# Performance work log

Hardware: AMD Instinct MI355X
Metric: run time of the kernel (lower is better)

The kernel has to match this reference:

```python
import jax, jax.numpy as jnp
import numpy as np

D_MODEL = 256
NCODES = 32


def setup_inputs() -> dict:
    key = jax.random.key(0)
    k1, k2 = jax.random.split(key)
    B, L = 64, 2048
    rev_repr = jax.random.normal(k1, (B, L, D_MODEL), dtype=jnp.float32)
    # xavier_normal for Linear(256 -> ncodes): std = sqrt(2/(fan_in+fan_out))
    std = (2.0 / (D_MODEL + NCODES)) ** 0.5
    W_codes = jax.random.normal(k2, (NCODES, D_MODEL), dtype=jnp.float32) * std
    return {"rev_repr": rev_repr, "W_codes": W_codes}


def reference(rev_repr, W_codes):
    # scores: (B, L, ncodes) = rev_repr @ W_codes.T
    scores = jnp.einsum('bld,kd->blk', rev_repr, W_codes)
    # softmax over the L (sequence) dimension, dim=1
    wts = jax.nn.softmax(scores, axis=1)
    # fused weighted-sum pooling: (B, ncodes, 256) — avoids (B,L,ncodes,256) intermediate
    contexts = jnp.einsum('blk,bld->bkd', wts, rev_repr)
    return contexts
```

## Files before the change

### kernel.cpp

```cpp
#include <hip/hip_runtime.h>
#include <math.h>

#define BATCH 64
#define LSEQ 2048
#define DMOD 256
#define KC 32
#define LCHUNK 128
#define NCH 16
#define LS 32
#define NSUB 4
#define PD 264
#define PT 40
#define PP 36

typedef __bf16 bf16x4 __attribute__((ext_vector_type(4)));
typedef __bf16 bf16x8 __attribute__((ext_vector_type(8)));
typedef float f32x4 __attribute__((ext_vector_type(4)));

union FragU {
  uint4 u;
  uint2 h[2];
  bf16x8 b;
};

__global__ __launch_bounds__(256, 4) void fused_pool_kernel(
    const float* __restrict__ rev, const float* __restrict__ W,
    float* __restrict__ cPartial, float* __restrict__ zPartial) {
  __shared__ __align__(16) __bf16 sRev[LS * PD];
  __shared__ __align__(16) __bf16 sRevT[DMOD * PT];
  __shared__ __align__(16) __bf16 sP[KC * PP];
  __shared__ float sZw[4][16];

  const int tid = threadIdx.x;
  const int b = blockIdx.y;
  const int lc = blockIdx.x;
  const int lbase = lc * LCHUNK;
  const int lane = tid & 63;
  const int wave = tid >> 6;
  const int col = lane & 15;
  const int quad = lane >> 4;
  const int Mt = wave & 1;
  const int Nt = wave >> 1;
  const int tp = tid & 127;
  const int th = tid >> 7;

  bf16x8 wfrag[8];
  {
    const float* wrow = W + (Nt * 16 + col) * DMOD + quad * 8;
#pragma unroll
    for (int ks = 0; ks < 8; ++ks) {
      float4 a = *(const float4*)(wrow + ks * 32);
      float4 c = *(const float4*)(wrow + ks * 32 + 4);
      bf16x8 f = {(__bf16)a.x, (__bf16)a.y, (__bf16)a.z, (__bf16)a.w,
                  (__bf16)c.x, (__bf16)c.y, (__bf16)c.z, (__bf16)c.w};
      wfrag[ks] = f;
    }
  }

  for (int rep = 0; rep < 2; ++rep) {
    f32x4 acc2[8];
#pragma unroll
    for (int i = 0; i < 8; ++i) acc2[i] = (f32x4){0.f, 0.f, 0.f, 0.f};
    float zl = 0.f;

#pragma unroll
    for (int i = 0; i < 8; ++i) {
      int slot = tid + 256 * i;
      int r = slot >> 6, c4 = slot & 63;
      float4 v = *(const float4*)(rev + ((size_t)b * LSEQ + lbase + r) * DMOD + c4 * 4);
      bf16x4 hh = {(__bf16)v.x, (__bf16)v.y, (__bf16)v.z, (__bf16)v.w};
      *(bf16x4*)(&sRev[r * PD + c4 * 4]) = hh;
    }
    __syncthreads();

    for (int sub = 0; sub < NSUB; ++sub) {
#pragma unroll
      for (int s2 = 0; s2 < 2; ++s2) {
        uint tmp[8];
#pragma unroll
        for (int j = 0; j < 8; ++j) {
          int ll = 16 * th + 8 * s2 + j;
          tmp[j] = *(const uint*)(&sRev[ll * PD + 2 * tp]);
        }
        uint lo[4], hi[4];
#pragma unroll
        for (int i = 0; i < 4; ++i) {
          lo[i] = (tmp[2 * i] & 0xffffu) | (tmp[2 * i + 1] << 16);
          hi[i] = (tmp[2 * i] >> 16) | (tmp[2 * i + 1] & 0xffff0000u);
        }
        uint4 vlo = {lo[0], lo[1], lo[2], lo[3]};
        uint4 vhi = {hi[0], hi[1], hi[2], hi[3]};
        *(uint4*)(&sRevT[(2 * tp) * PT + 16 * th + 8 * s2]) = vlo;
        *(uint4*)(&sRevT[(2 * tp + 1) * PT + 16 * th + 8 * s2]) = vhi;
      }

      f32x4 acc1 = {0.f, 0.f, 0.f, 0.f};
#pragma unroll
      for (int ks = 0; ks < 8; ++ks) {
        FragU af;
        af.u = *(const uint4*)(&sRev[(Mt * 16 + col) * PD + ks * 32 + quad * 8]);
        acc1 = __builtin_amdgcn_mfma_f32_16x16x32_bf16(af.b, wfrag[ks], acc1, 0, 0, 0);
      }
      {
        bf16x4 ph;
#pragma unroll
        for (int reg = 0; reg < 4; ++reg) {
          float p = __expf(acc1[reg]);
          ph[reg] = (__bf16)p;
          zl += (float)ph[reg];
        }
        *(bf16x4*)(&sP[(Nt * 16 + col) * PP + Mt * 16 + quad * 4]) = ph;
      }
      __syncthreads();

      FragU pa;
      pa.h[0] = *(const uint2*)(&sP[(Mt * 16 + col) * PP + quad * 8]);
      pa.h[1] = *(const uint2*)(&sP[(Mt * 16 + col) * PP + quad * 8 + 4]);
#pragma unroll
      for (int nt = 0; nt < 8; ++nt) {
        int d = (Nt * 8 + nt) * 16 + col;
        FragU bb;
        bb.u = *(const uint4*)(&sRevT[d * PT + quad * 8]);
        acc2[nt] = __builtin_amdgcn_mfma_f32_16x16x32_bf16(pa.b, bb.b, acc2[nt], 0, 0, 0);
      }
      if (sub + 1 < NSUB) {
        const int l1 = lbase + (sub + 1) * LS;
#pragma unroll
        for (int i = 0; i < 8; ++i) {
          int slot = tid + 256 * i;
          int r = slot >> 6, c4 = slot & 63;
          float4 v = *(const float4*)(rev + ((size_t)b * LSEQ + l1 + r) * DMOD + c4 * 4);
          bf16x4 hh = {(__bf16)v.x, (__bf16)v.y, (__bf16)v.z, (__bf16)v.w};
          *(bf16x4*)(&sRev[r * PD + c4 * 4]) = hh;
        }
        __syncthreads();
      }
    }

    float zz = zl;
    zz += __shfl_xor(zz, 16, 64);
    zz += __shfl_xor(zz, 32, 64);
    if (quad == 0) sZw[wave][col] = zz;
    __syncthreads();
    if (tid < KC) {
      int Ntt = tid >> 4, c = tid & 15;
      zPartial[((size_t)b * NCH + lc) * KC + tid] = sZw[2 * Ntt][c] + sZw[2 * Ntt + 1][c];
    }
    float* dst = cPartial + (((size_t)b * NCH + lc) * KC) * DMOD;
#pragma unroll
    for (int nt = 0; nt < 8; ++nt) {
      int d = (Nt * 8 + nt) * 16 + col;
#pragma unroll
      for (int reg = 0; reg < 4; ++reg) {
        int k = Mt * 16 + quad * 4 + reg;
        dst[k * DMOD + d] = acc2[nt][reg];
      }
    }
    __syncthreads();
  }
}

__global__ __launch_bounds__(256) void reduce_kernel(
    const float* __restrict__ cPartial, const float* __restrict__ zPartial,
    float* __restrict__ out) {
  int idx = blockIdx.x * 256 + threadIdx.x;
  int b = idx >> 11;
  int k = (idx >> 6) & 31;
  float4 s = {0.f, 0.f, 0.f, 0.f};
  float z = 0.f;
#pragma unroll
  for (int lcc = 0; lcc < NCH; ++lcc) {
    const float4 v = *(const float4*)(cPartial +
                                      ((((size_t)b * NCH + lcc) * KC + k) << 8) +
                                      ((idx & 63) << 2));
    s.x += v.x; s.y += v.y; s.z += v.z; s.w += v.w;
    z += zPartial[((size_t)b * NCH + lcc) * KC + k];
  }
  float zi = 1.0f / z;
  float4 o = {s.x * zi, s.y * zi, s.z * zi, s.w * zi};
  *(float4*)(out + ((size_t)idx << 2)) = o;
}

extern "C" void kernel_launch(void* const* d_in, const int* in_sizes, int n_in,
                              void* d_out, int out_size, void* d_ws,
                              size_t ws_size, hipStream_t stream) {
  const float* rev = (const float*)d_in[0];
  const float* W = (const float*)d_in[1];
  float* out = (float*)d_out;

  float* ws = (float*)d_ws;
  float* cPartial = ws;
  float* zPartial = cPartial + (size_t)BATCH * NCH * KC * DMOD;

  fused_pool_kernel<<<dim3(NCH, BATCH), dim3(256), 0, stream>>>(rev, W, cPartial,
                                                                zPartial);
  reduce_kernel<<<dim3(512), dim3(256), 0, stream>>>(cPartial, zPartial, out);
}
```

Before: 233.0 us.

## Use 512-thread blocks with 64-row subtiles and halve partial chunks

The fused pooling kernel now runs 512-thread blocks that each process a 256-row L chunk as four 64-row subtiles, instead of 256-thread blocks looping twice over 128-row chunks. The wave-to-tile mapping is reworked: 8 waves compute the scores tile, and the context MFMA now takes a K=64 reduction in two steps per output tile. NCH drops from 16 to 8, which halves the partial-sum writes and the work in the reduce kernel. In exchange it uses more shared memory and registers per block and launches fewer, larger blocks, which may lower occupancy.

```diff
diff --git a/kernel.cpp b/kernel.cpp
--- a/kernel.cpp
+++ b/kernel.cpp
@@ -5,13 +5,13 @@
 #define LSEQ 2048
 #define DMOD 256
 #define KC 32
-#define LCHUNK 128
-#define NCH 16
-#define LS 32
+#define LCH 256
+#define NCH 8
+#define LS 64
 #define NSUB 4
 #define PD 264
-#define PT 40
-#define PP 36
+#define PT 72
+#define PP 72
 
 typedef __bf16 bf16x4 __attribute__((ext_vector_type(4)));
 typedef __bf16 bf16x8 __attribute__((ext_vector_type(8)));
@@ -23,30 +23,32 @@
   bf16x8 b;
 };
 
-__global__ __launch_bounds__(256, 4) void fused_pool_kernel(
+__global__ __launch_bounds__(512, 4) void fused_pool_kernel(
     const float* __restrict__ rev, const float* __restrict__ W,
     float* __restrict__ cPartial, float* __restrict__ zPartial) {
   __shared__ __align__(16) __bf16 sRev[LS * PD];
   __shared__ __align__(16) __bf16 sRevT[DMOD * PT];
   __shared__ __align__(16) __bf16 sP[KC * PP];
-  __shared__ float sZw[4][16];
+  __shared__ float sZw[8][16];
 
   const int tid = threadIdx.x;
   const int b = blockIdx.y;
   const int lc = blockIdx.x;
-  const int lbase = lc * LCHUNK;
+  const int lbase = lc * LCH;
   const int lane = tid & 63;
   const int wave = tid >> 6;
   const int col = lane & 15;
   const int quad = lane >> 4;
-  const int Mt = wave & 1;
-  const int Nt = wave >> 1;
+  const int Mt1 = wave & 3;
+  const int Nt1 = wave >> 2;
+  const int Mt2 = wave & 1;
+  const int Dt = wave >> 1;
   const int tp = tid & 127;
   const int th = tid >> 7;
 
   bf16x8 wfrag[8];
   {
-    const float* wrow = W + (Nt * 16 + col) * DMOD + quad * 8;
+    const float* wrow = W + (Nt1 * 16 + col) * DMOD + quad * 8;
 #pragma unroll
     for (int ks = 0; ks < 8; ++ks) {
       float4 a = *(const float4*)(wrow + ks * 32);
@@ -57,106 +59,108 @@
     }
   }
 
-  for (int rep = 0; rep < 2; ++rep) {
-    f32x4 acc2[8];
-#pragma unroll
-    for (int i = 0; i < 8; ++i) acc2[i] = (f32x4){0.f, 0.f, 0.f, 0.f};
-    float zl = 0.f;
-
-#pragma unroll
-    for (int i = 0; i < 8; ++i) {
-      int slot = tid + 256 * i;
-      int r = slot >> 6, c4 = slot & 63;
-      float4 v = *(const float4*)(rev + ((size_t)b * LSEQ + lbase + r) * DMOD + c4 * 4);
-      bf16x4 hh = {(__bf16)v.x, (__bf16)v.y, (__bf16)v.z, (__bf16)v.w};
-      *(bf16x4*)(&sRev[r * PD + c4 * 4]) = hh;
+  f32x4 acc2[4];
+#pragma unroll
+  for (int i = 0; i < 4; ++i) acc2[i] = (f32x4){0.f, 0.f, 0.f, 0.f};
+  float zl = 0.f;
+
+#pragma unroll
+  for (int i = 0; i < 8; ++i) {
+    int slot = tid + 512 * i;
+    int r = slot >> 6, c4 = slot & 63;
+    float4 v = *(const float4*)(rev + ((size_t)b * LSEQ + lbase + r) * DMOD + c4 * 4);
+    bf16x4 hh = {(__bf16)v.x, (__bf16)v.y, (__bf16)v.z, (__bf16)v.w};
+    *(bf16x4*)(&sRev[r * PD + c4 * 4]) = hh;
+  }
+  __syncthreads();
+
+  for (int sub = 0; sub < NSUB; ++sub) {
+#pragma unroll
+    for (int s2 = 0; s2 < 2; ++s2) {
+      uint tmp[8];
+#pragma unroll
+      for (int j = 0; j < 8; ++j) {
+        int ll = 16 * th + 8 * s2 + j;
+        tmp[j] = *(const uint*)(&sRev[ll * PD + 2 * tp]);
+      }
+      uint lo[4], hi[4];
+#pragma unroll
+      for (int i = 0; i < 4; ++i) {
+        lo[i] = (tmp[2 * i] & 0xffffu) | (tmp[2 * i + 1] << 16);
+        hi[i] = (tmp[2 * i] >> 16) | (tmp[2 * i + 1] & 0xffff0000u);
+      }
+      uint4 vlo = {lo[0], lo[1], lo[2], lo[3]};
+      uint4 vhi = {hi[0], hi[1], hi[2], hi[3]};
+      *(uint4*)(&sRevT[(2 * tp) * PT + 16 * th + 8 * s2]) = vlo;
+      *(uint4*)(&sRevT[(2 * tp + 1) * PT + 16 * th + 8 * s2]) = vhi;
+    }
+
+    f32x4 acc1 = {0.f, 0.f, 0.f, 0.f};
+#pragma unroll
+    for (int ks = 0; ks < 8; ++ks) {
+      FragU af;
+      af.u = *(const uint4*)(&sRev[(Mt1 * 16 + col) * PD + ks * 32 + quad * 8]);
+      acc1 = __builtin_amdgcn_mfma_f32_16x16x32_bf16(af.b, wfrag[ks], acc1, 0, 0, 0);
+    }
+    {
+      bf16x4 ph;
+#pragma unroll
+      for (int reg = 0; reg < 4; ++reg) {
+        float p = __expf(acc1[reg]);
+        ph[reg] = (__bf16)p;
+        zl += (float)ph[reg];
+      }
+      *(bf16x4*)(&sP[(Nt1 * 16 + col) * PP + Mt1 * 16 + quad * 4]) = ph;
     }
     __syncthreads();
 
-    for (int sub = 0; sub < NSUB; ++sub) {
-#pragma unroll
-      for (int s2 = 0; s2 < 2; ++s2) {
-        uint tmp[8];
-#pragma unroll
-        for (int j = 0; j < 8; ++j) {
-          int ll = 16 * th + 8 * s2 + j;
-          tmp[j] = *(const uint*)(&sRev[ll * PD + 2 * tp]);
-        }
-        uint lo[4], hi[4];
-#pragma unroll
-        for (int i = 0; i < 4; ++i) {
-          lo[i] = (tmp[2 * i] & 0xffffu) | (tmp[2 * i + 1] << 16);
-          hi[i] = (tmp[2 * i] >> 16) | (tmp[2 * i + 1] & 0xffff0000u);
-        }
-        uint4 vlo = {lo[0], lo[1], lo[2], lo[3]};
-        uint4 vhi = {hi[0], hi[1], hi[2], hi[3]};
-        *(uint4*)(&sRevT[(2 * tp) * PT + 16 * th + 8 * s2]) = vlo;
-        *(uint4*)(&sRevT[(2 * tp + 1) * PT + 16 * th + 8 * s2]) = vhi;
-      }
-
-      f32x4 acc1 = {0.f, 0.f, 0.f, 0.f};
-#pragma unroll
-      for (int ks = 0; ks < 8; ++ks) {
-        FragU af;
-        af.u = *(const uint4*)(&sRev[(Mt * 16 + col) * PD + ks * 32 + quad * 8]);
-        acc1 = __builtin_amdgcn_mfma_f32_16x16x32_bf16(af.b, wfrag[ks], acc1, 0, 0, 0);
-      }
-      {
-        bf16x4 ph;
-#pragma unroll
-        for (int reg = 0; reg < 4; ++reg) {
-          float p = __expf(acc1[reg]);
-          ph[reg] = (__bf16)p;
-          zl += (float)ph[reg];
-        }
-        *(bf16x4*)(&sP[(Nt * 16 + col) * PP + Mt * 16 + quad * 4]) = ph;
+    FragU pa[2];
+#pragma unroll
+    for (int s = 0; s < 2; ++s)
+      pa[s].u = *(const uint4*)(&sP[(Mt2 * 16 + col) * PP + s * 32 + quad * 8]);
+#pragma unroll
+    for (int t = 0; t < 4; ++t) {
+      int drow = (Dt * 4 + t) * 16 + col;
+#pragma unroll
+      for (int s = 0; s < 2; ++s) {
+        FragU bb;
+        bb.u = *(const uint4*)(&sRevT[drow * PT + s * 32 + quad * 8]);
+        acc2[t] = __builtin_amdgcn_mfma_f32_16x16x32_bf16(pa[s].b, bb.b, acc2[t], 0, 0, 0);
+      }
+    }
+    if (sub + 1 < NSUB) {
+      const int l1 = lbase + (sub + 1) * LS;
+#pragma unroll
+      for (int i = 0; i < 8; ++i) {
+        int slot = tid + 512 * i;
+        int r = slot >> 6, c4 = slot & 63;
+        float4 v = *(const float4*)(rev + ((size_t)b * LSEQ + l1 + r) * DMOD + c4 * 4);
+        bf16x4 hh = {(__bf16)v.x, (__bf16)v.y, (__bf16)v.z, (__bf16)v.w};
+        *(bf16x4*)(&sRev[r * PD + c4 * 4]) = hh;
       }
       __syncthreads();
-
-      FragU pa;
-      pa.h[0] = *(const uint2*)(&sP[(Mt * 16 + col) * PP + quad * 8]);
-      pa.h[1] = *(const uint2*)(&sP[(Mt * 16 + col) * PP + quad * 8 + 4]);
-#pragma unroll
-      for (int nt = 0; nt < 8; ++nt) {
-        int d = (Nt * 8 + nt) * 16 + col;
-        FragU bb;
-        bb.u = *(const uint4*)(&sRevT[d * PT + quad * 8]);
-        acc2[nt] = __builtin_amdgcn_mfma_f32_16x16x32_bf16(pa.b, bb.b, acc2[nt], 0, 0, 0);
-      }
-      if (sub + 1 < NSUB) {
-        const int l1 = lbase + (sub + 1) * LS;
-#pragma unroll
-        for (int i = 0; i < 8; ++i) {
-          int slot = tid + 256 * i;
-          int r = slot >> 6, c4 = slot & 63;
-          float4 v = *(const float4*)(rev + ((size_t)b * LSEQ + l1 + r) * DMOD + c4 * 4);
-          bf16x4 hh = {(__bf16)v.x, (__bf16)v.y, (__bf16)v.z, (__bf16)v.w};
-          *(bf16x4*)(&sRev[r * PD + c4 * 4]) = hh;
-        }
-        __syncthreads();
-      }
-    }
-
-    float zz = zl;
-    zz += __shfl_xor(zz, 16, 64);
-    zz += __shfl_xor(zz, 32, 64);
-    if (quad == 0) sZw[wave][col] = zz;
-    __syncthreads();
-    if (tid < KC) {
-      int Ntt = tid >> 4, c = tid & 15;
-      zPartial[((size_t)b * NCH + lc) * KC + tid] = sZw[2 * Ntt][c] + sZw[2 * Ntt + 1][c];
-    }
-    float* dst = cPartial + (((size_t)b * NCH + lc) * KC) * DMOD;
-#pragma unroll
-    for (int nt = 0; nt < 8; ++nt) {
-      int d = (Nt * 8 + nt) * 16 + col;
-#pragma unroll
-      for (int reg = 0; reg < 4; ++reg) {
-        int k = Mt * 16 + quad * 4 + reg;
-        dst[k * DMOD + d] = acc2[nt][reg];
-      }
-    }
-    __syncthreads();
+    }
+  }
+
+  zl += __shfl_xor(zl, 16, 64);
+  zl += __shfl_xor(zl, 32, 64);
+  if (quad == 0) sZw[wave][col] = zl;
+  __syncthreads();
+  if (tid < KC) {
+    int h = tid >> 4, c = tid & 15;
+    zPartial[((size_t)b * NCH + lc) * KC + tid] =
+        sZw[h * 4 + 0][c] + sZw[h * 4 + 1][c] + sZw[h * 4 + 2][c] + sZw[h * 4 + 3][c];
+  }
+
+  float* dst = cPartial + (((size_t)b * NCH + lc) * KC) * DMOD;
+#pragma unroll
+  for (int t = 0; t < 4; ++t) {
+    int d = (Dt * 4 + t) * 16 + col;
+#pragma unroll
+    for (int reg = 0; reg < 4; ++reg) {
+      int k = Mt2 * 16 + quad * 4 + reg;
+      dst[k * DMOD + d] = acc2[t][reg];
+    }
   }
 }
 
@@ -192,7 +196,7 @@
   float* cPartial = ws;
   float* zPartial = cPartial + (size_t)BATCH * NCH * KC * DMOD;
 
-  fused_pool_kernel<<<dim3(NCH, BATCH), dim3(256), 0, stream>>>(rev, W, cPartial,
+  fused_pool_kernel<<<dim3(NCH, BATCH), dim3(512), 0, stream>>>(rev, W, cPartial,
                                                                 zPartial);
   reduce_kernel<<<dim3(512), dim3(256), 0, stream>>>(cPartial, zPartial, out);
 }
```

Result: faster. 197.1 us (-15.4%).
